# Performance work log

Hardware: AMD Instinct MI355X
Metric: run time of the kernel (lower is better)

## Reference

```python
import jax, jax.numpy as jnp
import numpy as np

B, C, L, D = 8, 32, 2048, 128
R, H = 8, 4  # num_routers, num_heads


def setup_inputs() -> dict:
    key = jax.random.key(0)
    ks = jax.random.split(key, 20)
    p = lambda k, shape: jax.random.normal(k, shape, dtype=jnp.float32) * 0.02
    inp = {
        "Z": jax.random.normal(ks[0], (B, C, L, D), dtype=jnp.float32),
        "router": p(ks[1], (R, D)),
        # router_sender projections (d_model -> d_model, torch Linear stored as x@W+b)
        "Wq1": p(ks[2], (D, D)), "bq1": jnp.zeros((D,), jnp.float32),
        "Wk1": p(ks[3], (D, D)), "bk1": jnp.zeros((D,), jnp.float32),
        "Wv1": p(ks[4], (D, D)), "bv1": jnp.zeros((D,), jnp.float32),
        "Wo1": p(ks[5], (D, D)), "bo1": jnp.zeros((D,), jnp.float32),
        # router_receiver projections
        "Wq2": p(ks[6], (D, D)), "bq2": jnp.zeros((D,), jnp.float32),
        "Wk2": p(ks[7], (D, D)), "bk2": jnp.zeros((D,), jnp.float32),
        "Wv2": p(ks[8], (D, D)), "bv2": jnp.zeros((D,), jnp.float32),
        "Wo2": p(ks[9], (D, D)), "bo2": jnp.zeros((D,), jnp.float32),
        # LayerNorm
        "gamma": jnp.ones((D,), jnp.float32),
        "beta": jnp.zeros((D,), jnp.float32),
    }
    return inp


def _cross_attn(q_in, k_in, v_in, Wq, bq, Wk, bk, Wv, bv, Wo, bo):
    # Informer FullAttention + AttentionLayer (dropout=0)
    Bn, Lq, Dm = q_in.shape
    Lk = k_in.shape[1]
    dh = Dm // H
    q = (q_in @ Wq + bq).reshape(Bn, Lq, H, dh)
    k = (k_in @ Wk + bk).reshape(Bn, Lk, H, dh)
    v = (v_in @ Wv + bv).reshape(Bn, Lk, H, dh)
    scale = 1.0 / np.sqrt(dh)
    scores = jnp.einsum("blhe,bshe->bhls", q, k) * scale
    A = jax.nn.softmax(scores, axis=-1)
    out = jnp.einsum("bhls,bshd->blhd", A, v).reshape(Bn, Lq, Dm)
    return out @ Wo + bo


def _layernorm(x, gamma, beta, eps=1e-5):
    mu = jnp.mean(x, axis=-1, keepdims=True)
    var = jnp.mean(jnp.square(x - mu), axis=-1, keepdims=True)
    return (x - mu) * jax.lax.rsqrt(var + eps) * gamma + beta


def reference(Z, router, Wq1, bq1, Wk1, bk1, Wv1, bv1, Wo1, bo1,
              Wq2, bq2, Wk2, bk2, Wv2, bv2, Wo2, bo2, gamma, beta):
    Bz, Cz, Lz, Dz = Z.shape
    x = Z.reshape(Bz * Cz, Lz, Dz)
    batch_router = jnp.broadcast_to(router[None], (Bz * Cz, R, Dz))
    # stage 1: routers attend to the sequence (R x L)
    router_buffer = _cross_attn(batch_router, x, x,
                                Wq1, bq1, Wk1, bk1, Wv1, bv1, Wo1, bo1)
    # stage 2: sequence attends to routers (L x R)
    router_receive = _cross_attn(x, router_buffer, router_buffer,
                                 Wq2, bq2, Wk2, bk2, Wv2, bv2, Wo2, bo2)
    out = _layernorm(x + router_receive, gamma, beta)
    return out.reshape(Bz, Cz, Lz, Dz)
```

## Files before the change

### kernel.cpp

```cpp
#include <hip/hip_runtime.h>

typedef float f4_t __attribute__((ext_vector_type(4)));
typedef __bf16 bf8_t __attribute__((ext_vector_type(8)));
typedef __bf16 bf4_t __attribute__((ext_vector_type(4)));

#define MFMA16(a,b,c) __builtin_amdgcn_mfma_f32_16x16x32_bf16((a),(b),(c),0,0,0)

static constexpr float kScale = 0.17677669529663687f;

__global__ __launch_bounds__(256) void k0_fold(
    const float* __restrict__ router, const float* __restrict__ Wq1,
    const float* __restrict__ bq1, const float* __restrict__ Wk1,
    const float* __restrict__ bk1, __bf16* __restrict__ q1t,
    float* __restrict__ c1)
{
  __shared__ float q1[8][128];
  const int t = threadIdx.x;
  for (int idx = t; idx < 1024; idx += 256) {
    int r = idx >> 7, dp = idx & 127;
    float acc = bq1[dp];
    for (int e = 0; e < 128; ++e) acc += router[r*128 + e] * Wq1[e*128 + dp];
    q1[r][dp] = acc;
  }
  __syncthreads();
  for (int idx = t; idx < 4096; idx += 256) {
    int j = idx >> 7, e = idx & 127;
    int h = j >> 3, r = j & 7;
    float acc = 0.f;
    for (int d = 0; d < 32; ++d) acc += q1[r][h*32 + d] * Wk1[e*128 + h*32 + d];
    q1t[idx] = (__bf16)(acc * kScale);
  }
  if (t < 32) {
    int h = t >> 3, r = t & 7;
    float acc = 0.f;
    for (int d = 0; d < 32; ++d) acc += q1[r][h*32 + d] * bk1[h*32 + d];
    c1[t] = acc * kScale;
  }
}

__global__ __launch_bounds__(512) void k1_stage1(
    const float* __restrict__ Z, const __bf16* __restrict__ q1t_g,
    const float* __restrict__ c1_g, float* __restrict__ xap,
    float* __restrict__ lp)
{
  __shared__ __bf16 xb[64][136];
  __shared__ __bf16 xT[128][72];
  __shared__ __bf16 PT[32][72];
  __shared__ __bf16 q1t[32][136];
  __shared__ float lds_l[32];

  const int tid = threadIdx.x;
  const int bid = blockIdx.x;
  const float* xbase = Z + (size_t)bid * (1024 * 128);

  {
    int j = tid >> 4, e0 = (tid & 15) << 3;
    *(uint4*)&q1t[j][e0] = *(const uint4*)(q1t_g + j*128 + e0);
  }
  if (tid < 32) lds_l[tid] = 0.f;

  const int lane = tid & 63;
  const int w = tid >> 6;
  const int lc = lane & 15;
  const int lg = lane >> 4;
  const int ms = w >> 2;
  const int ns = w & 3;
  float c1v[4];
#pragma unroll
  for (int r2 = 0; r2 < 4; ++r2) c1v[r2] = c1_g[ms*16 + lg*4 + r2];

  const f4_t fzero = {0.f, 0.f, 0.f, 0.f};
  f4_t accxa[2] = { fzero, fzero };
  float Lacc[4] = {0.f, 0.f, 0.f, 0.f};

  __syncthreads();

  for (int tile = 0; tile < 16; ++tile) {
    const float* xt = xbase + tile * (64 * 128);
#pragma unroll
    for (int i = 0; i < 4; ++i) {
      int f = tid + i*512;
      int pos = f >> 5, d0 = (f & 31) << 2;
      f4_t v = __builtin_nontemporal_load((const f4_t*)(xt + pos*128 + d0));
      bf4_t b4 = { (__bf16)v.x, (__bf16)v.y, (__bf16)v.z, (__bf16)v.w };
      *(bf4_t*)&xb[pos][d0] = b4;
    }
    __syncthreads();
#pragma unroll
    for (int s = 0; s < 2; ++s) {
      int u = tid + s*512;
      int dim = u & 127, pb = (u >> 7) << 3;
      bf8_t t8;
#pragma unroll
      for (int p = 0; p < 8; ++p) t8[p] = xb[pb + p][dim];
      *(bf8_t*)&xT[dim][pb] = t8;
    }
    f4_t sacc = fzero;
#pragma unroll
    for (int ks = 0; ks < 4; ++ks) {
      bf8_t a = *(const bf8_t*)&q1t[ms*16 + lc][ks*32 + lg*8];
      bf8_t b = *(const bf8_t*)&xb[ns*16 + lc][ks*32 + lg*8];
      sacc = MFMA16(a, b, sacc);
    }
    const int posn = ns*16 + lc;
#pragma unroll
    for (int r2 = 0; r2 < 4; ++r2) {
      float p = __expf(sacc[r2] + c1v[r2]);
      Lacc[r2] += p;
      PT[ms*16 + lg*4 + r2][posn] = (__bf16)p;
    }
    __syncthreads();
#pragma unroll
    for (int nt = 0; nt < 2; ++nt) {
      const int dimt = (ns << 1) + nt;
#pragma unroll
      for (int ks = 0; ks < 2; ++ks) {
        bf8_t a = *(const bf8_t*)&PT[ms*16 + lc][ks*32 + lg*8];
        bf8_t b = *(const bf8_t*)&xT[dimt*16 + lc][ks*32 + lg*8];
        accxa[nt] = MFMA16(a, b, accxa[nt]);
      }
    }
    __syncthreads();
  }

#pragma unroll
  for (int r2 = 0; r2 < 4; ++r2) {
    float v = Lacc[r2];
    v += __shfl_xor(v, 1);
    v += __shfl_xor(v, 2);
    v += __shfl_xor(v, 4);
    v += __shfl_xor(v, 8);
    if (lc == 0) atomicAdd(&lds_l[ms*16 + lg*4 + r2], v);
  }
  __syncthreads();

  float* xo = xap + (size_t)bid * 4096;
#pragma unroll
  for (int nt = 0; nt < 2; ++nt) {
    const int dim = ((ns << 1) + nt)*16 + lc;
#pragma unroll
    for (int r2 = 0; r2 < 4; ++r2) {
      int j = ms*16 + lg*4 + r2;
      xo[j*128 + dim] = accxa[nt][r2];
    }
  }
  if (tid < 32) lp[bid*32 + tid] = lds_l[tid];
}

__global__ __launch_bounds__(256) void k1b_mid(
    const float* __restrict__ xap, const float* __restrict__ lp,
    const float* __restrict__ Wv1, const float* __restrict__ bv1,
    const float* __restrict__ Wo1, const float* __restrict__ bo1,
    const float* __restrict__ Wk2, const float* __restrict__ bk2,
    const float* __restrict__ Wv2, const float* __restrict__ bv2,
    const float* __restrict__ Wq2, const float* __restrict__ bq2,
    const float* __restrict__ Wo2,
    __bf16* __restrict__ kt2, float* __restrict__ c2, __bf16* __restrict__ vt2)
{
  __shared__ float xa[32][129];
  __shared__ float invl[32];
  __shared__ float out1[8][128];
  __shared__ float rb[8][128];
  __shared__ float k2s[8][128];
  __shared__ float v2s[8][128];

  const int t = threadIdx.x, b = blockIdx.x;
  const float* p0 = xap + (size_t)(b*2) * 4096;
  const float* p1 = xap + (size_t)(b*2 + 1) * 4096;
  for (int idx = t; idx < 4096; idx += 256)
    xa[idx >> 7][idx & 127] = p0[idx] + p1[idx];
  if (t < 32) invl[t] = 1.f / (lp[b*64 + t] + lp[b*64 + 32 + t]);
  __syncthreads();

  for (int idx = t; idx < 1024; idx += 256) {
    int r = idx >> 7, hd = idx & 127, h = hd >> 5;
    int j = h*8 + r;
    float acc = 0.f;
    for (int e = 0; e < 128; ++e) acc += xa[j][e] * Wv1[e*128 + hd];
    out1[r][hd] = acc * invl[j] + bv1[hd];
  }
  __syncthreads();
  for (int idx = t; idx < 1024; idx += 256) {
    int r = idx >> 7, e2 = idx & 127;
    float acc = bo1[e2];
    for (int hd = 0; hd < 128; ++hd) acc += out1[r][hd] * Wo1[hd*128 + e2];
    rb[r][e2] = acc;
  }
  __syncthreads();
  for (int idx = t; idx < 2048; idx += 256) {
    int sel = idx >> 10;
    int r = (idx >> 7) & 7, hd = idx & 127;
    const float* W = sel ? Wv2 : Wk2;
    const float* bb = sel ? bv2 : bk2;
    float acc = bb[hd];
    for (int e = 0; e < 128; ++e) acc += rb[r][e] * W[e*128 + hd];
    float (*dst)[128] = sel ? v2s : k2s;
    dst[r][hd] = acc;
  }
  __syncthreads();
  for (int idx = t; idx < 4096; idx += 256) {
    int j = idx >> 7, e = idx & 127;
    int h = j >> 3, r = j & 7;
    float acck = 0.f, accv = 0.f;
    for (int d = 0; d < 32; ++d) {
      acck += Wq2[e*128 + h*32 + d] * k2s[r][h*32 + d];
      accv += v2s[r][h*32 + d] * Wo2[(h*32 + d)*128 + e];
    }
    kt2[(size_t)b*4096 + j*128 + e] = (__bf16)(acck * kScale);
    vt2[(size_t)b*4096 + e*32 + j] = (__bf16)accv;
  }
  if (t < 32) {
    int h = t >> 3, r = t & 7;
    float acc = 0.f;
    for (int d = 0; d < 32; ++d) acc += bq2[h*32 + d] * k2s[r][h*32 + d];
    c2[b*32 + t] = acc * kScale;
  }
}

__global__ __launch_bounds__(512) void k2_stage2(
    const float* __restrict__ Z, const __bf16* __restrict__ kt2,
    const float* __restrict__ c2g, const __bf16* __restrict__ vt2,
    const float* __restrict__ bo2, const float* __restrict__ gamma,
    const float* __restrict__ beta, float* __restrict__ out)
{
  __shared__ __bf16 xb[128][136];
  __shared__ __bf16 kt[32][136];
  __shared__ __bf16 vT[128][56];
  __shared__ __bf16 P2[128][56];

  const int tid = threadIdx.x;
  const int bid = blockIdx.x;
  const int batch = bid >> 4;
  const size_t rowbase = (size_t)bid * (128 * 128);
  const float* x = Z + rowbase;
  float* y = out + rowbase;

  {
    int j = tid >> 4, e0 = (tid & 15) << 3;
    *(uint4*)&kt[j][e0] = *(const uint4*)(kt2 + (size_t)batch*4096 + j*128 + e0);
  }
  {
    int e = tid >> 2, j0 = (tid & 3) << 3;
    *(uint4*)&vT[e][j0] = *(const uint4*)(vt2 + (size_t)batch*4096 + e*32 + j0);
  }
  f4_t zv[8];
#pragma unroll
  for (int i = 0; i < 8; ++i) {
    int f = tid + i*512;
    int pos = f >> 5, d0 = (f & 31) << 2;
    zv[i] = __builtin_nontemporal_load((const f4_t*)(x + pos*128 + d0));
  }
#pragma unroll
  for (int i = 0; i < 8; ++i) {
    int f = tid + i*512;
    int pos = f >> 5, d0 = (f & 31) << 2;
    bf4_t b4 = { (__bf16)zv[i].x, (__bf16)zv[i].y, (__bf16)zv[i].z, (__bf16)zv[i].w };
    *(bf4_t*)&xb[pos][d0] = b4;
  }
  __syncthreads();

  const int lane = tid & 63;
  const int w = tid >> 6;
  const int lc = lane & 15;
  const int lg = lane >> 4;

  const f4_t fzero = {0.f, 0.f, 0.f, 0.f};

  f4_t sacc[2] = { fzero, fzero };
#pragma unroll
  for (int ks = 0; ks < 4; ++ks) {
    bf8_t a = *(const bf8_t*)&xb[w*16 + lc][ks*32 + lg*8];
#pragma unroll
    for (int nt = 0; nt < 2; ++nt) {
      bf8_t b = *(const bf8_t*)&kt[nt*16 + lc][ks*32 + lg*8];
      sacc[nt] = MFMA16(a, b, sacc[nt]);
    }
  }
  float c2v[2] = { c2g[batch*32 + lc], c2g[batch*32 + 16 + lc] };
#pragma unroll
  for (int nt = 0; nt < 2; ++nt) {
#pragma unroll
    for (int r2 = 0; r2 < 4; ++r2) {
      float s = sacc[nt][r2] + c2v[nt];
      float m = s;
      m = fmaxf(m, __shfl_xor(m, 1));
      m = fmaxf(m, __shfl_xor(m, 2));
      m = fmaxf(m, __shfl_xor(m, 4));
      float p = __expf(s - m);
      float sum = p;
      sum += __shfl_xor(sum, 1);
      sum += __shfl_xor(sum, 2);
      sum += __shfl_xor(sum, 4);
      P2[w*16 + lg*4 + r2][nt*16 + lc] = (__bf16)(p / sum);
    }
  }
  __syncthreads();

  bf8_t pa = *(const bf8_t*)&P2[w*16 + lc][lg*8];
  f4_t racc[8];
#pragma unroll
  for (int nt = 0; nt < 8; ++nt) {
    bf8_t b = *(const bf8_t*)&vT[nt*16 + lc][lg*8];
    racc[nt] = MFMA16(pa, b, fzero);
  }

  float bo2v[8], gv[8], bv[8];
#pragma unroll
  for (int nt = 0; nt < 8; ++nt) {
    int dd = nt*16 + lc;
    bo2v[nt] = bo2[dd]; gv[nt] = gamma[dd]; bv[nt] = beta[dd];
  }
#pragma unroll
  for (int r2 = 0; r2 < 4; ++r2) {
    int pos = w*16 + lg*4 + r2;
    float vv[8];
    float s1 = 0.f, s2 = 0.f;
#pragma unroll
    for (int nt = 0; nt < 8; ++nt) {
      float xv = (float)xb[pos][nt*16 + lc];
      float tv = racc[nt][r2] + bo2v[nt] + xv;
      vv[nt] = tv; s1 += tv; s2 += tv*tv;
    }
    s1 += __shfl_xor(s1, 1); s1 += __shfl_xor(s1, 2);
    s1 += __shfl_xor(s1, 4); s1 += __shfl_xor(s1, 8);
    s2 += __shfl_xor(s2, 1); s2 += __shfl_xor(s2, 2);
    s2 += __shfl_xor(s2, 4); s2 += __shfl_xor(s2, 8);
    float mean = s1 * (1.f/128.f);
    float var = s2 * (1.f/128.f) - mean*mean;
    float rstd = rsqrtf(var + 1e-5f);
#pragma unroll
    for (int nt = 0; nt < 8; ++nt)
      __builtin_nontemporal_store((vv[nt] - mean) * rstd * gv[nt] + bv[nt],
                                  &y[pos*128 + nt*16 + lc]);
  }
}

extern "C" void kernel_launch(void* const* d_in, const int* in_sizes, int n_in,
                              void* d_out, int out_size, void* d_ws, size_t ws_size,
                              hipStream_t stream)
{
  const float* Z     = (const float*)d_in[0];
  const float* router= (const float*)d_in[1];
  const float* Wq1   = (const float*)d_in[2];
  const float* bq1   = (const float*)d_in[3];
  const float* Wk1   = (const float*)d_in[4];
  const float* bk1   = (const float*)d_in[5];
  const float* Wv1   = (const float*)d_in[6];
  const float* bv1   = (const float*)d_in[7];
  const float* Wo1   = (const float*)d_in[8];
  const float* bo1   = (const float*)d_in[9];
  const float* Wq2   = (const float*)d_in[10];
  const float* bq2   = (const float*)d_in[11];
  const float* Wk2   = (const float*)d_in[12];
  const float* bk2   = (const float*)d_in[13];
  const float* Wv2   = (const float*)d_in[14];
  const float* bv2   = (const float*)d_in[15];
  const float* Wo2   = (const float*)d_in[16];
  const float* bo2   = (const float*)d_in[17];
  const float* gamma = (const float*)d_in[18];
  const float* beta  = (const float*)d_in[19];
  float* out = (float*)d_out;

  char* base = (char*)d_ws;
  __bf16* q1tb = (__bf16*)base;
  float*  c1   = (float*)(base + 8192);
  float*  c2   = (float*)(base + 8448);
  float*  lp   = (float*)(base + 41216);
  float*  xap  = (float*)(base + 131072);
  __bf16* kt2b = (__bf16*)(base + 131072 + 8388608);
  __bf16* vt2b = (__bf16*)(base + 131072 + 8388608 + 2097152);
  (void)in_sizes; (void)n_in; (void)out_size; (void)ws_size;

  k0_fold<<<dim3(1), dim3(256), 0, stream>>>(router, Wq1, bq1, Wk1, bk1, q1tb, c1);
  k1_stage1<<<dim3(512), dim3(512), 0, stream>>>(Z, q1tb, c1, xap, lp);
  k1b_mid<<<dim3(256), dim3(256), 0, stream>>>(xap, lp, Wv1, bv1, Wo1, bo1,
                                               Wk2, bk2, Wv2, bv2, Wq2, bq2, Wo2,
                                               kt2b, c2, vt2b);
  k2_stage2<<<dim3(4096), dim3(512), 0, stream>>>(Z, kt2b, c2, vt2b, bo2, gamma, beta, out);
}
```

Before: 298.8 us.

## Stream Z directly into MFMA operands and drop LDS staging in stage 2

The stage-2 kernel now uses 64-row tiles with 256 threads. Each wave loads its own Z rows from global memory, converts them to bf16 in registers and feeds them straight into the score MFMA, and also writes them to LDS for the residual step. The K and V operands are read directly from global memory instead of being staged through shared memory, and both block-wide barriers are removed because each wave only touches its own rows. This is meant to cut LDS traffic, barrier stalls and shared-memory footprint so more blocks fit per CU. In exchange the Z loads are no longer nontemporal and fully coalesced in the old pattern, and K/V are re-read per wave through cache.

Result: slower. 321.4 us (+7.6%).

```diff
diff --git a/kernel.cpp b/kernel.cpp
--- a/kernel.cpp
+++ b/kernel.cpp
@@ -217,62 +217,45 @@
   }
 }
 
-__global__ __launch_bounds__(512) void k2_stage2(
+__global__ __launch_bounds__(256, 4) void k2_stage2(
     const float* __restrict__ Z, const __bf16* __restrict__ kt2,
     const float* __restrict__ c2g, const __bf16* __restrict__ vt2,
     const float* __restrict__ bo2, const float* __restrict__ gamma,
     const float* __restrict__ beta, float* __restrict__ out)
 {
-  __shared__ __bf16 xb[128][136];
-  __shared__ __bf16 kt[32][136];
-  __shared__ __bf16 vT[128][56];
-  __shared__ __bf16 P2[128][56];
+  __shared__ __bf16 xb[64][136];
+  __shared__ __bf16 P2[64][56];
 
   const int tid = threadIdx.x;
   const int bid = blockIdx.x;
-  const int batch = bid >> 4;
-  const size_t rowbase = (size_t)bid * (128 * 128);
+  const int batch = bid >> 5;
+  const size_t rowbase = (size_t)bid * (64 * 128);
   const float* x = Z + rowbase;
   float* y = out + rowbase;
 
-  {
-    int j = tid >> 4, e0 = (tid & 15) << 3;
-    *(uint4*)&kt[j][e0] = *(const uint4*)(kt2 + (size_t)batch*4096 + j*128 + e0);
-  }
-  {
-    int e = tid >> 2, j0 = (tid & 3) << 3;
-    *(uint4*)&vT[e][j0] = *(const uint4*)(vt2 + (size_t)batch*4096 + e*32 + j0);
-  }
-  f4_t zv[8];
-#pragma unroll
-  for (int i = 0; i < 8; ++i) {
-    int f = tid + i*512;
-    int pos = f >> 5, d0 = (f & 31) << 2;
-    zv[i] = __builtin_nontemporal_load((const f4_t*)(x + pos*128 + d0));
-  }
-#pragma unroll
-  for (int i = 0; i < 8; ++i) {
-    int f = tid + i*512;
-    int pos = f >> 5, d0 = (f & 31) << 2;
-    bf4_t b4 = { (__bf16)zv[i].x, (__bf16)zv[i].y, (__bf16)zv[i].z, (__bf16)zv[i].w };
-    *(bf4_t*)&xb[pos][d0] = b4;
-  }
-  __syncthreads();
+  const __bf16* ktb = kt2 + (size_t)batch * 4096;
+  const __bf16* vtb = vt2 + (size_t)batch * 4096;
 
   const int lane = tid & 63;
   const int w = tid >> 6;
   const int lc = lane & 15;
   const int lg = lane >> 4;
+  const int arow = w*16 + lc;
 
   const f4_t fzero = {0.f, 0.f, 0.f, 0.f};
 
   f4_t sacc[2] = { fzero, fzero };
 #pragma unroll
   for (int ks = 0; ks < 4; ++ks) {
-    bf8_t a = *(const bf8_t*)&xb[w*16 + lc][ks*32 + lg*8];
+    const float* xp = x + arow*128 + ks*32 + lg*8;
+    f4_t v0 = *(const f4_t*)xp;
+    f4_t v1 = *(const f4_t*)(xp + 4);
+    bf8_t a = { (__bf16)v0.x, (__bf16)v0.y, (__bf16)v0.z, (__bf16)v0.w,
+                (__bf16)v1.x, (__bf16)v1.y, (__bf16)v1.z, (__bf16)v1.w };
+    *(bf8_t*)&xb[arow][ks*32 + lg*8] = a;
 #pragma unroll
     for (int nt = 0; nt < 2; ++nt) {
-      bf8_t b = *(const bf8_t*)&kt[nt*16 + lc][ks*32 + lg*8];
+      bf8_t b = *(const bf8_t*)(ktb + (nt*16 + lc)*128 + ks*32 + lg*8);
       sacc[nt] = MFMA16(a, b, sacc[nt]);
     }
   }
@@ -294,13 +277,12 @@
       P2[w*16 + lg*4 + r2][nt*16 + lc] = (__bf16)(p / sum);
     }
   }
-  __syncthreads();
 
   bf8_t pa = *(const bf8_t*)&P2[w*16 + lc][lg*8];
   f4_t racc[8];
 #pragma unroll
   for (int nt = 0; nt < 8; ++nt) {
-    bf8_t b = *(const bf8_t*)&vT[nt*16 + lc][lg*8];
+    bf8_t b = *(const bf8_t*)(vtb + (nt*16 + lc)*32 + lg*8);
     racc[nt] = MFMA16(pa, b, fzero);
   }
 
@@ -376,5 +358,5 @@
   k1b_mid<<<dim3(256), dim3(256), 0, stream>>>(xap, lp, Wv1, bv1, Wo1, bo1,
                                                Wk2, bk2, Wv2, bv2, Wq2, bq2, Wo2,
                                                kt2b, c2, vt2b);
-  k2_stage2<<<dim3(4096), dim3(512), 0, stream>>>(Z, kt2b, c2, vt2b, bo2, gamma, beta, out);
-}
+  k2_stage2<<<dim3(8192), dim3(256), 0, stream>>>(Z, kt2b, c2, vt2b, bo2, gamma, beta, out);
+}
```
